# Kernel tuning notes

Hardware: AMD Instinct MI355X
Metric: run time of the kernel (lower is better)

Reference implementation:

```python
import jax, jax.numpy as jnp
import numpy as np

N, NFEAT, NHID, NCLASS = 8192, 128, 128, 40


def _init(key, shape, fan_in):
    return jax.random.normal(key, shape, jnp.float32) / np.sqrt(fan_in).astype(np.float32)


def setup_inputs() -> dict:
    ks = jax.random.split(jax.random.key(0), 8)
    return {
        "x": jax.random.normal(ks[0], (N, NFEAT), jnp.float32),
        # dense normalized adjacency: row-stochastic-ish positive matrix
        "adj": jax.random.uniform(ks[1], (N, N), jnp.float32) * (2.0 / N),
        "W_emb": _init(ks[2], (NFEAT, NHID), NFEAT),
        "b_emb": jnp.zeros((NHID,), jnp.float32),
        "W_gc1": _init(ks[3], (NHID, NHID), NHID),
        "b_gc1": jnp.zeros((NHID,), jnp.float32),
        "W_e": _init(ks[4], (2 * NHID, NHID), 2 * NHID),
        "b_e": jnp.zeros((NHID,), jnp.float32),
        "W_gc2": _init(ks[5], (NHID, NCLASS), NHID),
        "b_gc2": jnp.zeros((NCLASS,), jnp.float32),
        "fully_connected_graph": 1,  # unused by forward (passed but never read)
    }


def reference(x, adj, W_emb, b_emb, W_gc1, b_gc1, W_e, b_e, W_gc2, b_gc2,
              fully_connected_graph):
    nhid = W_emb.shape[1]
    # x = self.emb(x)
    h = x @ W_emb + b_emb  # [N, nhid]

    # Edge branch. Original materializes edge_feat[i*N+j] = concat(h[i], h[j])
    # ([N*N, 2*nhid]) then GraphConvolution_edge: support = edge_feat @ W_e,
    # reshaped [N, N, nhid], aggregated x_e[i] = sum_j adj[i,j] * support[i,j] + b_e.
    # Algebraically identical fused form (same math, no O(N^2*nhid) tensor):
    #   support[i,j] = h[i] @ W_e[:nhid] + h[j] @ W_e[nhid:]
    #   x_e[i] = deg[i] * (h[i] @ W_e_src) + (adj @ (h @ W_e_dst))[i] + b_e
    s_src = h @ W_e[:nhid]   # [N, nhid]
    s_dst = h @ W_e[nhid:]   # [N, nhid]
    deg = adj.sum(axis=1, keepdims=True)  # [N, 1] row sums
    x_e = deg * s_src + adj @ s_dst + b_e  # [N, nhid]

    # Node branch: gc1 -> relu -> dropout(eval: identity) -> gc2 -> log_softmax
    h1 = jax.nn.relu(adj @ (h @ W_gc1) + b_gc1)       # [N, nhid]
    logits = adj @ (h1 @ W_gc2) + b_gc2               # [N, nclass]
    out = jax.nn.log_softmax(logits, axis=1)
    return out, x_e
```

## Files before the change

### kernel.cpp

```cpp
#include <hip/hip_runtime.h>

#define DI __device__ __forceinline__

using f32x4  = __attribute__((ext_vector_type(4))) float;
using bf16x8 = __attribute__((ext_vector_type(8))) __bf16;
using u16x4  = __attribute__((ext_vector_type(4))) unsigned short;
using u32x4  = __attribute__((ext_vector_type(4))) unsigned int;

constexpr int NNODE = 8192;

DI unsigned short f2bf(float f) {
    unsigned int u = __builtin_bit_cast(unsigned int, f);
    u += 0x7fffu + ((u >> 16) & 1u);
    return (unsigned short)(u >> 16);
}
DI float bf2f(unsigned short s) {
    return __builtin_bit_cast(float, (unsigned int)s << 16);
}

DI int swz256(int r, int cb) { return r * 256 + (cb ^ ((r & 15) << 4)); }
DI int swz128(int r, int cb) { return r * 128 + (cb ^ ((r & 7) << 4)); }

__global__ void prep_w(const float* __restrict__ W_emb, const float* __restrict__ W_e,
                       const float* __restrict__ W_gc1, const float* __restrict__ W_gc2,
                       unsigned short* __restrict__ WembT_hi, unsigned short* __restrict__ WembT_lo,
                       unsigned short* __restrict__ WcatT_hi, unsigned short* __restrict__ WcatT_lo,
                       unsigned short* __restrict__ Wg2T_hi, unsigned short* __restrict__ Wg2T_lo)
{
    int gid = blockIdx.x * 256 + threadIdx.x;
    if (gid >= 576 * 128) return;
    int k = gid & 127, n = gid >> 7;
    float v;
    unsigned short *dh, *dl;
    if (n < 128) {
        v = W_emb[k * 128 + n];
        dh = WembT_hi + n * 128 + k; dl = WembT_lo + n * 128 + k;
    } else if (n < 512) {
        int m = n - 128;
        if (m < 128)      v = W_e[k * 128 + m];
        else if (m < 256) v = W_e[(k + 128) * 128 + (m - 128)];
        else              v = W_gc1[k * 128 + (m - 256)];
        dh = WcatT_hi + m * 128 + k; dl = WcatT_lo + m * 128 + k;
    } else {
        int c = n - 512;
        v = (c < 40) ? W_gc2[k * 40 + c] : 0.f;
        dh = Wg2T_hi + c * 128 + k; dl = Wg2T_lo + c * 128 + k;
    }
    unsigned short hi = f2bf(v);
    *dh = hi;
    *dl = f2bf(v - bf2f(hi));
}

__global__ __launch_bounds__(512) void gemm_hs(
    const float* __restrict__ x,
    const unsigned short* __restrict__ WembT_hi, const unsigned short* __restrict__ WembT_lo,
    const unsigned short* __restrict__ WcatT_hi, const unsigned short* __restrict__ WcatT_lo,
    const float* __restrict__ b_emb,
    float* __restrict__ out_s,
    unsigned short* __restrict__ out_t)
{
    __shared__ unsigned short Hh[64 * 128], Hl[64 * 128];
    char* Hhc = (char*)Hh; char* Hlc = (char*)Hl;

    const int tid = threadIdx.x;
    const int r0 = blockIdx.x * 64;
    const int lane = tid & 63, wid = tid >> 6;
    const int lrow = lane & 15, lk8 = (lane >> 4) * 8, lkb = (lane >> 4) * 16;
    const int wrg = wid & 3;
    const int wcg = wid >> 2;

    #pragma unroll
    for (int p = 0; p < 4; ++p) {
        int idx = tid + 512 * p, r = idx >> 5, c4 = idx & 31;
        f32x4 v = *(const f32x4*)(x + (size_t)(r0 + r) * 128 + c4 * 4);
        u16x4 ph, pl;
        #pragma unroll
        for (int j = 0; j < 4; ++j) {
            unsigned short hi = f2bf(v[j]);
            ph[j] = hi; pl[j] = f2bf(v[j] - bf2f(hi));
        }
        *(u16x4*)(Hhc + swz256(r, c4 * 8)) = ph;
        *(u16x4*)(Hlc + swz256(r, c4 * 8)) = pl;
    }
    __syncthreads();

    f32x4 acc[4];
    #pragma unroll
    for (int i = 0; i < 4; ++i) acc[i] = f32x4{0.f, 0.f, 0.f, 0.f};
    const int arow = wrg * 16 + lrow;
    #pragma unroll
    for (int kk = 0; kk < 4; ++kk) {
        bf16x8 ah = *(const bf16x8*)(Hhc + swz256(arow, kk * 64 + lkb));
        bf16x8 al = *(const bf16x8*)(Hlc + swz256(arow, kk * 64 + lkb));
        #pragma unroll
        for (int nf = 0; nf < 4; ++nf) {
            const int n = wcg * 64 + nf * 16 + lrow;
            bf16x8 bh = *(const bf16x8*)(WembT_hi + (size_t)n * 128 + kk * 32 + lk8);
            bf16x8 bl = *(const bf16x8*)(WembT_lo + (size_t)n * 128 + kk * 32 + lk8);
            acc[nf] = __builtin_amdgcn_mfma_f32_16x16x32_bf16(ah, bh, acc[nf], 0, 0, 0);
            acc[nf] = __builtin_amdgcn_mfma_f32_16x16x32_bf16(ah, bl, acc[nf], 0, 0, 0);
            acc[nf] = __builtin_amdgcn_mfma_f32_16x16x32_bf16(al, bh, acc[nf], 0, 0, 0);
        }
    }
    __syncthreads();

    #pragma unroll
    for (int nf = 0; nf < 4; ++nf) {
        const int col = wcg * 64 + nf * 16 + lrow;
        const float bv = b_emb[col];
        #pragma unroll
        for (int j = 0; j < 4; ++j) {
            const int row = wrg * 16 + ((lane >> 4) << 2) + j;
            float v = acc[nf][j] + bv;
            unsigned short hi = f2bf(v);
            *(unsigned short*)(Hhc + swz256(row, col * 2)) = hi;
            *(unsigned short*)(Hlc + swz256(row, col * 2)) = f2bf(v - bf2f(hi));
        }
    }
    __syncthreads();

    f32x4 acc2[12];
    #pragma unroll
    for (int i = 0; i < 12; ++i) acc2[i] = f32x4{0.f, 0.f, 0.f, 0.f};
    #pragma unroll
    for (int kk = 0; kk < 4; ++kk) {
        bf16x8 ah = *(const bf16x8*)(Hhc + swz256(arow, kk * 64 + lkb));
        bf16x8 al = *(const bf16x8*)(Hlc + swz256(arow, kk * 64 + lkb));
        #pragma unroll
        for (int nf = 0; nf < 12; ++nf) {
            const int n = wcg * 192 + nf * 16 + lrow;
            bf16x8 bh = *(const bf16x8*)(WcatT_hi + (size_t)n * 128 + kk * 32 + lk8);
            bf16x8 bl = *(const bf16x8*)(WcatT_lo + (size_t)n * 128 + kk * 32 + lk8);
            acc2[nf] = __builtin_amdgcn_mfma_f32_16x16x32_bf16(ah, bh, acc2[nf], 0, 0, 0);
            acc2[nf] = __builtin_amdgcn_mfma_f32_16x16x32_bf16(ah, bl, acc2[nf], 0, 0, 0);
            acc2[nf] = __builtin_amdgcn_mfma_f32_16x16x32_bf16(al, bh, acc2[nf], 0, 0, 0);
        }
    }
    const int rowb = r0 + wrg * 16 + ((lane >> 4) << 2);
    #pragma unroll
    for (int nf = 0; nf < 12; ++nf) {
        const int col = wcg * 192 + nf * 16 + lrow;
        if (wcg == 0 && nf < 8) {
            #pragma unroll
            for (int j = 0; j < 4; ++j)
                out_s[(size_t)(rowb + j) * 128 + col] = acc2[nf][j];
        } else {
            u16x4 pk = { f2bf(acc2[nf][0]), f2bf(acc2[nf][1]), f2bf(acc2[nf][2]), f2bf(acc2[nf][3]) };
            *(u16x4*)(out_t + (size_t)(col - 128) * NNODE + rowb) = pk;
        }
    }
}

template<int NCOLS, int KSPLIT, bool DEG, bool REV>
__global__ __launch_bounds__(512) void adj_gemm(
    const float* __restrict__ adj,
    const unsigned short* __restrict__ Bt,
    float* __restrict__ Tpart,
    float* __restrict__ degp)
{
    __shared__ unsigned short A_lds[2][64 * 64];
    __shared__ unsigned short B_lds[2][NCOLS * 64];

    const int tid = threadIdx.x;
    const int r0 = blockIdx.x * 64;
    const int ks = blockIdx.y;
    constexpr int KLEN = NNODE / KSPLIT;
    constexpr int NT = KLEN / 64;
    const int kbase = ks * KLEN;

    constexpr int NB = NCOLS / 64;
    f32x4 areg[2];
    u32x4 breg[NB];
    float dsum0 = 0.f, dsum1 = 0.f;
    const int ar0 = tid >> 4, ac4 = tid & 15;

    const int lane = tid & 63, wid = tid >> 6;
    constexpr int FM = (NCOLS == 256) ? 2 : 1;
    constexpr int FN = (NCOLS == 256) ? 4 : 2;
    const int wr = (NCOLS == 256) ? (wid >> 2) : (wid >> 1);
    const int wc = (NCOLS == 256) ? (wid & 3) : (wid & 1);
    const int row_w = wr * FM * 16, col_w = wc * FN * 16;
    const int lrow = lane & 15, lkb = (lane >> 4) * 16;

    f32x4 acc[FM][FN];
    #pragma unroll
    for (int fm = 0; fm < FM; ++fm)
        #pragma unroll
        for (int fn = 0; fn < FN; ++fn) acc[fm][fn] = f32x4{0.f, 0.f, 0.f, 0.f};

    auto order = [&](int tt) { return REV ? (NT - 1 - tt) : tt; };

    auto loadG = [&](int t) {
        const int kt = kbase + t * 64;
        #pragma unroll
        for (int p = 0; p < 2; ++p) {
            areg[p] = *(const f32x4*)(adj + (size_t)(r0 + ar0 + 32 * p) * NNODE + kt + ac4 * 4);
            if (DEG) {
                float s = areg[p][0] + areg[p][1] + areg[p][2] + areg[p][3];
                if (p == 0) dsum0 += s; else dsum1 += s;
            }
        }
        #pragma unroll
        for (int p = 0; p < NB; ++p) {
            const int idx = tid + 512 * p, n = idx >> 3, c = idx & 7;
            breg[p] = *(const u32x4*)(Bt + (size_t)n * NNODE + kt + c * 8);
        }
    };
    auto storeL = [&](int buf) {
        char* Ac = (char*)(A_lds[buf]);
        char* Bc = (char*)(B_lds[buf]);
        #pragma unroll
        for (int p = 0; p < 2; ++p) {
            u16x4 pk = { f2bf(areg[p][0]), f2bf(areg[p][1]), f2bf(areg[p][2]), f2bf(areg[p][3]) };
            *(u16x4*)(Ac + swz128(ar0 + 32 * p, ac4 * 8)) = pk;
        }
        #pragma unroll
        for (int p = 0; p < NB; ++p) {
            const int idx = tid + 512 * p, n = idx >> 3, c = idx & 7;
            *(u32x4*)(Bc + swz128(n, c * 16)) = breg[p];
        }
    };

    loadG(order(0));
    storeL(0);
    for (int tt = 0; tt < NT; ++tt) {
        if (tt + 1 < NT) loadG(order(tt + 1));
        __syncthreads();
        const char* Ac = (const char*)(A_lds[tt & 1]);
        const char* Bc = (const char*)(B_lds[tt & 1]);
        #pragma unroll
        for (int kk = 0; kk < 2; ++kk) {
            bf16x8 a[FM], b[FN];
            #pragma unroll
            for (int fm = 0; fm < FM; ++fm)
                a[fm] = *(const bf16x8*)(Ac + swz128(row_w + fm * 16 + lrow, kk * 64 + lkb));
            #pragma unroll
            for (int fn = 0; fn < FN; ++fn)
                b[fn] = *(const bf16x8*)(Bc + swz128(col_w + fn * 16 + lrow, kk * 64 + lkb));
            #pragma unroll
            for (int fm = 0; fm < FM; ++fm)
                #pragma unroll
                for (int fn = 0; fn < FN; ++fn)
                    acc[fm][fn] = __builtin_amdgcn_mfma_f32_16x16x32_bf16(a[fm], b[fn], acc[fm][fn], 0, 0, 0);
        }
        if (tt + 1 < NT) storeL((tt + 1) & 1);
    }

    float* outp = Tpart + (size_t)ks * NNODE * NCOLS;
    #pragma unroll
    for (int fm = 0; fm < FM; ++fm) {
        const int grow0 = r0 + row_w + fm * 16 + ((lane >> 4) << 2);
        #pragma unroll
        for (int fn = 0; fn < FN; ++fn) {
            const int gcol = col_w + fn * 16 + lrow;
            #pragma unroll
            for (int j = 0; j < 4; ++j)
                outp[(size_t)(grow0 + j) * NCOLS + gcol] = acc[fm][fn][j];
        }
    }

    if (DEG) {
        __syncthreads();
        float* sc = (float*)(&A_lds[0][0]);
        sc[tid] = dsum0;
        sc[512 + tid] = dsum1;
        __syncthreads();
        if (tid < 64) {
            const int base = (tid < 32) ? tid * 16 : (512 + (tid - 32) * 16);
            float s = 0.f;
            #pragma unroll
            for (int i = 0; i < 16; ++i) s += sc[base + i];
            degp[(size_t)ks * NNODE + r0 + tid] = s;
        }
    }
}

template<int KSA>
__global__ __launch_bounds__(256) void post1g2(
    const float* __restrict__ tA,
    const float* __restrict__ s_src,
    const float* __restrict__ degp,
    const float* __restrict__ b_e,
    const float* __restrict__ b_gc1,
    const unsigned short* __restrict__ Wg2T_hi, const unsigned short* __restrict__ Wg2T_lo,
    float* __restrict__ x_e_out,
    unsigned short* __restrict__ out_t)
{
    __shared__ unsigned short Hh[64 * 128], Hl[64 * 128];
    char* Hhc = (char*)Hh; char* Hlc = (char*)Hl;

    const int tid = threadIdx.x;
    const int r0 = blockIdx.x * 64;

    #pragma unroll
    for (int p = 0; p < 8; ++p) {
        int idx = tid + 256 * p, r = idx >> 5, c4 = idx & 31;
        const int gi = r0 + r;
        float dv = 0.f;
        #pragma unroll
        for (int q = 0; q < KSA; ++q) dv += degp[(size_t)q * NNODE + gi];
        f32x4 sdst = f32x4{0.f, 0.f, 0.f, 0.f}, g1 = f32x4{0.f, 0.f, 0.f, 0.f};
        #pragma unroll
        for (int q = 0; q < KSA; ++q) {
            const float* tp = tA + (size_t)q * NNODE * 256 + (size_t)gi * 256;
            f32x4 a = *(const f32x4*)(tp + c4 * 4);
            f32x4 b = *(const f32x4*)(tp + 128 + c4 * 4);
            #pragma unroll
            for (int j = 0; j < 4; ++j) { sdst[j] += a[j]; g1[j] += b[j]; }
        }
        f32x4 ss = *(const f32x4*)(s_src + (size_t)gi * 128 + c4 * 4);
        f32x4 be = *(const f32x4*)(b_e + c4 * 4);
        f32x4 bg = *(const f32x4*)(b_gc1 + c4 * 4);
        f32x4 xe;
        u16x4 ph, pl;
        #pragma unroll
        for (int j = 0; j < 4; ++j) {
            xe[j] = dv * ss[j] + sdst[j] + be[j];
            float h1 = g1[j] + bg[j];
            h1 = h1 > 0.f ? h1 : 0.f;
            unsigned short hi = f2bf(h1);
            ph[j] = hi; pl[j] = f2bf(h1 - bf2f(hi));
        }
        *(f32x4*)(x_e_out + (size_t)gi * 128 + c4 * 4) = xe;
        *(u16x4*)(Hhc + swz256(r, c4 * 8)) = ph;
        *(u16x4*)(Hlc + swz256(r, c4 * 8)) = pl;
    }
    __syncthreads();

    const int lane = tid & 63, wid = tid >> 6;
    const int lrow = lane & 15, lk8 = (lane >> 4) * 8, lkb = (lane >> 4) * 16;
    f32x4 acc[4];
    #pragma unroll
    for (int i = 0; i < 4; ++i) acc[i] = f32x4{0.f, 0.f, 0.f, 0.f};
    const int arow = wid * 16 + lrow;
    #pragma unroll
    for (int kk = 0; kk < 4; ++kk) {
        bf16x8 ah = *(const bf16x8*)(Hhc + swz256(arow, kk * 64 + lkb));
        bf16x8 al = *(const bf16x8*)(Hlc + swz256(arow, kk * 64 + lkb));
        #pragma unroll
        for (int nf = 0; nf < 4; ++nf) {
            const int n = nf * 16 + lrow;
            bf16x8 bh = *(const bf16x8*)(Wg2T_hi + (size_t)n * 128 + kk * 32 + lk8);
            bf16x8 bl = *(const bf16x8*)(Wg2T_lo + (size_t)n * 128 + kk * 32 + lk8);
            acc[nf] = __builtin_amdgcn_mfma_f32_16x16x32_bf16(ah, bh, acc[nf], 0, 0, 0);
            acc[nf] = __builtin_amdgcn_mfma_f32_16x16x32_bf16(ah, bl, acc[nf], 0, 0, 0);
            acc[nf] = __builtin_amdgcn_mfma_f32_16x16x32_bf16(al, bh, acc[nf], 0, 0, 0);
        }
    }
    const int rowb = r0 + wid * 16 + ((lane >> 4) << 2);
    #pragma unroll
    for (int nf = 0; nf < 4; ++nf) {
        const int col = nf * 16 + lrow;
        u16x4 pk = { f2bf(acc[nf][0]), f2bf(acc[nf][1]), f2bf(acc[nf][2]), f2bf(acc[nf][3]) };
        *(u16x4*)(out_t + (size_t)col * NNODE + rowb) = pk;
    }
}

template<int KSPLIT>
__global__ void logsm(const float* __restrict__ tB,
                      const float* __restrict__ b_gc2,
                      float* __restrict__ out)
{
    const int wid = threadIdx.x >> 6, lane = threadIdx.x & 63;
    const int row = blockIdx.x * 4 + wid;
    float v = -1e30f;
    if (lane < 40) {
        float s = b_gc2[lane];
        #pragma unroll
        for (int p = 0; p < KSPLIT; ++p)
            s += tB[(size_t)p * NNODE * 64 + (size_t)row * 64 + lane];
        v = s;
    }
    float m = v;
    #pragma unroll
    for (int off = 32; off; off >>= 1) m = fmaxf(m, __shfl_xor(m, off, 64));
    float e = (lane < 40) ? expf(v - m) : 0.f;
    float s = e;
    #pragma unroll
    for (int off = 32; off; off >>= 1) s += __shfl_xor(s, off, 64);
    if (lane < 40) out[(size_t)row * 40 + lane] = v - m - logf(s);
}

extern "C" void kernel_launch(void* const* d_in, const int* in_sizes, int n_in,
                              void* d_out, int out_size, void* d_ws, size_t ws_size,
                              hipStream_t stream)
{
    const float* x     = (const float*)d_in[0];
    const float* adj   = (const float*)d_in[1];
    const float* W_emb = (const float*)d_in[2];
    const float* b_emb = (const float*)d_in[3];
    const float* W_gc1 = (const float*)d_in[4];
    const float* b_gc1 = (const float*)d_in[5];
    const float* W_e   = (const float*)d_in[6];
    const float* b_e   = (const float*)d_in[7];
    const float* W_gc2 = (const float*)d_in[8];
    const float* b_gc2 = (const float*)d_in[9];

    constexpr int KSA = 2;
    constexpr int KSB = 2;

    char* p = (char*)d_ws;
    auto take = [&](size_t bytes) { char* q = p; p += (bytes + 255) & ~(size_t)255; return q; };

    unsigned short* WembT_hi = (unsigned short*)take(128 * 128 * 2);
    unsigned short* WembT_lo = (unsigned short*)take(128 * 128 * 2);
    unsigned short* WcatT_hi = (unsigned short*)take(384 * 128 * 2);
    unsigned short* WcatT_lo = (unsigned short*)take(384 * 128 * 2);
    unsigned short* Wg2T_hi  = (unsigned short*)take(64 * 128 * 2);
    unsigned short* Wg2T_lo  = (unsigned short*)take(64 * 128 * 2);
    float*          s_src    = (float*)take((size_t)NNODE * 128 * 4);
    unsigned short* B_A      = (unsigned short*)take((size_t)256 * NNODE * 2);
    unsigned short* B_B      = (unsigned short*)take((size_t)64 * NNODE * 2);
    float*          tA       = (float*)take((size_t)KSA * NNODE * 256 * 4);
    float*          tB       = (float*)take((size_t)KSB * NNODE * 64 * 4);
    float*          degp     = (float*)take((size_t)KSA * NNODE * 4);

    float* out_ls = (float*)d_out;
    float* x_e    = (float*)d_out + (size_t)NNODE * 40;

    prep_w<<<288, 256, 0, stream>>>(W_emb, W_e, W_gc1, W_gc2,
                                    WembT_hi, WembT_lo, WcatT_hi, WcatT_lo, Wg2T_hi, Wg2T_lo);
    gemm_hs<<<128, 512, 0, stream>>>(x, WembT_hi, WembT_lo, WcatT_hi, WcatT_lo, b_emb,
                                     s_src, B_A);
    adj_gemm<256, KSA, true, false><<<dim3(128, KSA), 512, 0, stream>>>(adj, B_A, tA, degp);
    post1g2<KSA><<<128, 256, 0, stream>>>(tA, s_src, degp, b_e, b_gc1,
                                          Wg2T_hi, Wg2T_lo, x_e, B_B);
    adj_gemm<64, KSB, false, true><<<dim3(128, KSB), 512, 0, stream>>>(adj, B_B, tB, nullptr);
    logsm<KSB><<<2048, 256, 0, stream>>>(tB, b_gc2, out_ls);
}
```

Baseline: 163.7 us.

## Double register prefetch in adj GEMM with LDS-only barrier

Global loads for the adj GEMM now fill two alternating register sets, so two tiles are in flight instead of one, and the loop is unrolled by two across the LDS double buffer. `__syncthreads` is replaced by a barrier that waits only on LDS counters (`lgkmcnt`), so outstanding global loads are not drained at each barrier. The degree row-sum moves from load time to LDS-store time. This is meant to hide global-memory latency better, at the cost of more vector registers and an assumption that the tile count is even.

New measurement: 174.0 us. 1.06x slower.

```diff
diff --git a/kernel.cpp b/kernel.cpp
--- a/kernel.cpp
+++ b/kernel.cpp
@@ -16,6 +16,12 @@
 }
 DI float bf2f(unsigned short s) {
     return __builtin_bit_cast(float, (unsigned int)s << 16);
+}
+
+DI void lbar() {
+    asm volatile("s_waitcnt lgkmcnt(0)" ::: "memory");
+    __builtin_amdgcn_s_barrier();
+    asm volatile("" ::: "memory");
 }
 
 DI int swz256(int r, int cb) { return r * 256 + (cb ^ ((r & 15) << 4)); }
@@ -169,8 +175,8 @@
     const int kbase = ks * KLEN;
 
     constexpr int NB = NCOLS / 64;
-    f32x4 areg[2];
-    u32x4 breg[NB];
+    struct Regs { f32x4 a[2]; u32x4 b[NB]; };
+    Regs R0, R1;
     float dsum0 = 0.f, dsum1 = 0.f;
     const int ar0 = tid >> 4, ac4 = tid & 15;
 
@@ -190,44 +196,38 @@
 
     auto order = [&](int tt) { return REV ? (NT - 1 - tt) : tt; };
 
-    auto loadG = [&](int t) {
-        const int kt = kbase + t * 64;
+    auto loadG = [&](int t, Regs& R) {
+        const int kt = kbase + order(t) * 64;
+        #pragma unroll
+        for (int p = 0; p < 2; ++p)
+            R.a[p] = *(const f32x4*)(adj + (size_t)(r0 + ar0 + 32 * p) * NNODE + kt + ac4 * 4);
+        #pragma unroll
+        for (int p = 0; p < NB; ++p) {
+            const int idx = tid + 512 * p, n = idx >> 3, c = idx & 7;
+            R.b[p] = *(const u32x4*)(Bt + (size_t)n * NNODE + kt + c * 8);
+        }
+    };
+    auto storeL = [&](int buf, Regs& R) {
+        char* Ac = (char*)(A_lds[buf]);
+        char* Bc = (char*)(B_lds[buf]);
         #pragma unroll
         for (int p = 0; p < 2; ++p) {
-            areg[p] = *(const f32x4*)(adj + (size_t)(r0 + ar0 + 32 * p) * NNODE + kt + ac4 * 4);
             if (DEG) {
-                float s = areg[p][0] + areg[p][1] + areg[p][2] + areg[p][3];
+                float s = R.a[p][0] + R.a[p][1] + R.a[p][2] + R.a[p][3];
                 if (p == 0) dsum0 += s; else dsum1 += s;
             }
+            u16x4 pk = { f2bf(R.a[p][0]), f2bf(R.a[p][1]), f2bf(R.a[p][2]), f2bf(R.a[p][3]) };
+            *(u16x4*)(Ac + swz128(ar0 + 32 * p, ac4 * 8)) = pk;
         }
         #pragma unroll
         for (int p = 0; p < NB; ++p) {
             const int idx = tid + 512 * p, n = idx >> 3, c = idx & 7;
-            breg[p] = *(const u32x4*)(Bt + (size_t)n * NNODE + kt + c * 8);
+            *(u32x4*)(Bc + swz128(n, c * 16)) = R.b[p];
         }
     };
-    auto storeL = [&](int buf) {
-        char* Ac = (char*)(A_lds[buf]);
-        char* Bc = (char*)(B_lds[buf]);
-        #pragma unroll
-        for (int p = 0; p < 2; ++p) {
-            u16x4 pk = { f2bf(areg[p][0]), f2bf(areg[p][1]), f2bf(areg[p][2]), f2bf(areg[p][3]) };
-            *(u16x4*)(Ac + swz128(ar0 + 32 * p, ac4 * 8)) = pk;
-        }
-        #pragma unroll
-        for (int p = 0; p < NB; ++p) {
-            const int idx = tid + 512 * p, n = idx >> 3, c = idx & 7;
-            *(u32x4*)(Bc + swz128(n, c * 16)) = breg[p];
-        }
-    };
-
-    loadG(order(0));
-    storeL(0);
-    for (int tt = 0; tt < NT; ++tt) {
-        if (tt + 1 < NT) loadG(order(tt + 1));
-        __syncthreads();
-        const char* Ac = (const char*)(A_lds[tt & 1]);
-        const char* Bc = (const char*)(B_lds[tt & 1]);
+    auto compute = [&](int buf) {
+        const char* Ac = (const char*)(A_lds[buf]);
+        const char* Bc = (const char*)(B_lds[buf]);
         #pragma unroll
         for (int kk = 0; kk < 2; ++kk) {
             bf16x8 a[FM], b[FN];
@@ -243,7 +243,21 @@
                 for (int fn = 0; fn < FN; ++fn)
                     acc[fm][fn] = __builtin_amdgcn_mfma_f32_16x16x32_bf16(a[fm], b[fn], acc[fm][fn], 0, 0, 0);
         }
-        if (tt + 1 < NT) storeL((tt + 1) & 1);
+    };
+
+    loadG(0, R0);
+    loadG(1, R1);
+    storeL(0, R0);
+    lbar();
+    for (int t = 0; t < NT; t += 2) {
+        if (t + 2 < NT) loadG(t + 2, R0);
+        compute(0);
+        storeL(1, R1);
+        lbar();
+        if (t + 3 < NT) loadG(t + 3, R1);
+        compute(1);
+        if (t + 2 < NT) storeL(0, R0);
+        lbar();
     }
 
     float* outp = Tpart + (size_t)ks * NNODE * NCOLS;
```

## Use direct global-to-LDS async loads with triple buffering in adj GEMM

Applied to the files above, without the earlier changes.

Replaces the register-staged double-buffered load of adj and B tiles with __builtin_amdgcn_global_load_lds DMA into a three-stage LDS ring, issuing loads two tiles ahead and waiting with explicit vmcnt counts. The adj tile now stays in fp32 in LDS and is converted to bf16 at fragment-read time, and the degree row sums are computed from the LDS fragments and reduced with wave shuffles instead of a separate LDS reduction. The aim is to take VGPR staging and conversion off the load path and deepen the prefetch to hide HBM latency. In exchange, LDS use grows (fp32 A, three buffers), which may lower occupancy, and conversion work is repeated per MFMA wave.

After: 222.5 us. 1.36x slower.

```diff
diff --git a/kernel.cpp b/kernel.cpp
--- a/kernel.cpp
+++ b/kernel.cpp
@@ -9,6 +9,9 @@
 
 constexpr int NNODE = 8192;
 
+#define CAST_G(p) (const __attribute__((address_space(1))) unsigned int*)(p)
+#define CAST_S(p) (__attribute__((address_space(3))) unsigned int*)(p)
+
 DI unsigned short f2bf(float f) {
     unsigned int u = __builtin_bit_cast(unsigned int, f);
     u += 0x7fffu + ((u >> 16) & 1u);
@@ -20,6 +23,7 @@
 
 DI int swz256(int r, int cb) { return r * 256 + (cb ^ ((r & 15) << 4)); }
 DI int swz128(int r, int cb) { return r * 128 + (cb ^ ((r & 7) << 4)); }
+DI int swzA(int r, int cb)   { return r * 256 + (cb ^ ((r & 15) << 4)); }
 
 __global__ void prep_w(const float* __restrict__ W_emb, const float* __restrict__ W_e,
                        const float* __restrict__ W_gc1, const float* __restrict__ W_gc2,
@@ -158,98 +162,111 @@
     float* __restrict__ Tpart,
     float* __restrict__ degp)
 {
-    __shared__ unsigned short A_lds[2][64 * 64];
-    __shared__ unsigned short B_lds[2][NCOLS * 64];
+    __shared__ float A_lds[3][64 * 64];
+    __shared__ unsigned short B_lds[3][NCOLS * 64];
 
     const int tid = threadIdx.x;
+    const int lane = tid & 63, wid = tid >> 6;
     const int r0 = blockIdx.x * 64;
     const int ks = blockIdx.y;
     constexpr int KLEN = NNODE / KSPLIT;
     constexpr int NT = KLEN / 64;
     const int kbase = ks * KLEN;
 
-    constexpr int NB = NCOLS / 64;
-    f32x4 areg[2];
-    u32x4 breg[NB];
-    float dsum0 = 0.f, dsum1 = 0.f;
-    const int ar0 = tid >> 4, ac4 = tid & 15;
-
-    const int lane = tid & 63, wid = tid >> 6;
+    constexpr int NBA = 2;
+    constexpr int NBB = NCOLS / 64;
+    constexpr int VM = NBA + NBB;
+
     constexpr int FM = (NCOLS == 256) ? 2 : 1;
     constexpr int FN = (NCOLS == 256) ? 4 : 2;
     const int wr = (NCOLS == 256) ? (wid >> 2) : (wid >> 1);
     const int wc = (NCOLS == 256) ? (wid & 3) : (wid & 1);
     const int row_w = wr * FM * 16, col_w = wc * FN * 16;
-    const int lrow = lane & 15, lkb = (lane >> 4) * 16;
+    const int lrow = lane & 15, g4 = lane >> 4;
 
     f32x4 acc[FM][FN];
     #pragma unroll
     for (int fm = 0; fm < FM; ++fm)
         #pragma unroll
         for (int fn = 0; fn < FN; ++fn) acc[fm][fn] = f32x4{0.f, 0.f, 0.f, 0.f};
-
-    auto order = [&](int tt) { return REV ? (NT - 1 - tt) : tt; };
-
-    auto loadG = [&](int t) {
-        const int kt = kbase + t * 64;
-        #pragma unroll
-        for (int p = 0; p < 2; ++p) {
-            areg[p] = *(const f32x4*)(adj + (size_t)(r0 + ar0 + 32 * p) * NNODE + kt + ac4 * 4);
-            if (DEG) {
-                float s = areg[p][0] + areg[p][1] + areg[p][2] + areg[p][3];
-                if (p == 0) dsum0 += s; else dsum1 += s;
+    float dsum[FM];
+    #pragma unroll
+    for (int fm = 0; fm < FM; ++fm) dsum[fm] = 0.f;
+
+    auto dma = [&](int t, int buf) {
+        const int kt = kbase + (REV ? (NT - 1 - t) : t) * 64;
+        #pragma unroll
+        for (int p = 0; p < NBA; ++p) {
+            const int bidx = wid * 64 + 512 * p;
+            const int idx  = bidx + lane;
+            const int ra   = idx >> 4;
+            const int ce   = ((idx ^ (idx >> 4)) & 15) << 2;
+            __builtin_amdgcn_global_load_lds(
+                CAST_G(adj + (size_t)(r0 + ra) * NNODE + kt + ce),
+                CAST_S(&A_lds[buf][bidx * 4]), 16, 0, 0);
+        }
+        #pragma unroll
+        for (int p = 0; p < NBB; ++p) {
+            const int bidx = wid * 64 + 512 * p;
+            const int idx  = bidx + lane;
+            const int n    = idx >> 3;
+            const int ce   = ((idx ^ (idx >> 3)) & 7) << 3;
+            __builtin_amdgcn_global_load_lds(
+                CAST_G(Bt + (size_t)n * NNODE + kt + ce),
+                CAST_S(&B_lds[buf][bidx * 8]), 16, 0, 0);
+        }
+    };
+
+    auto compute = [&](int buf) {
+        const char* Ac = (const char*)(A_lds[buf]);
+        const char* Bc = (const char*)(B_lds[buf]);
+        #pragma unroll
+        for (int kk = 0; kk < 2; ++kk) {
+            bf16x8 a[FM];
+            #pragma unroll
+            for (int fm = 0; fm < FM; ++fm) {
+                const int r = row_w + fm * 16 + lrow;
+                const int cb0 = kk * 128 + g4 * 32;
+                f32x4 lo = *(const f32x4*)(Ac + swzA(r, cb0));
+                f32x4 hi = *(const f32x4*)(Ac + swzA(r, cb0 + 16));
+                #pragma unroll
+                for (int j = 0; j < 4; ++j) {
+                    a[fm][j]     = __builtin_bit_cast(__bf16, f2bf(lo[j]));
+                    a[fm][4 + j] = __builtin_bit_cast(__bf16, f2bf(hi[j]));
+                }
+                if (DEG && wc == 0)
+                    dsum[fm] += (lo[0] + lo[1] + lo[2] + lo[3]) + (hi[0] + hi[1] + hi[2] + hi[3]);
             }
-        }
-        #pragma unroll
-        for (int p = 0; p < NB; ++p) {
-            const int idx = tid + 512 * p, n = idx >> 3, c = idx & 7;
-            breg[p] = *(const u32x4*)(Bt + (size_t)n * NNODE + kt + c * 8);
-        }
-    };
-    auto storeL = [&](int buf) {
-        char* Ac = (char*)(A_lds[buf]);
-        char* Bc = (char*)(B_lds[buf]);
-        #pragma unroll
-        for (int p = 0; p < 2; ++p) {
-            u16x4 pk = { f2bf(areg[p][0]), f2bf(areg[p][1]), f2bf(areg[p][2]), f2bf(areg[p][3]) };
-            *(u16x4*)(Ac + swz128(ar0 + 32 * p, ac4 * 8)) = pk;
-        }
-        #pragma unroll
-        for (int p = 0; p < NB; ++p) {
-            const int idx = tid + 512 * p, n = idx >> 3, c = idx & 7;
-            *(u32x4*)(Bc + swz128(n, c * 16)) = breg[p];
-        }
-    };
-
-    loadG(order(0));
-    storeL(0);
-    for (int tt = 0; tt < NT; ++tt) {
-        if (tt + 1 < NT) loadG(order(tt + 1));
-        __syncthreads();
-        const char* Ac = (const char*)(A_lds[tt & 1]);
-        const char* Bc = (const char*)(B_lds[tt & 1]);
-        #pragma unroll
-        for (int kk = 0; kk < 2; ++kk) {
-            bf16x8 a[FM], b[FN];
-            #pragma unroll
-            for (int fm = 0; fm < FM; ++fm)
-                a[fm] = *(const bf16x8*)(Ac + swz128(row_w + fm * 16 + lrow, kk * 64 + lkb));
+            bf16x8 b[FN];
             #pragma unroll
             for (int fn = 0; fn < FN; ++fn)
-                b[fn] = *(const bf16x8*)(Bc + swz128(col_w + fn * 16 + lrow, kk * 64 + lkb));
+                b[fn] = *(const bf16x8*)(Bc + swz128(col_w + fn * 16 + lrow, kk * 64 + g4 * 16));
             #pragma unroll
             for (int fm = 0; fm < FM; ++fm)
                 #pragma unroll
                 for (int fn = 0; fn < FN; ++fn)
                     acc[fm][fn] = __builtin_amdgcn_mfma_f32_16x16x32_bf16(a[fm], b[fn], acc[fm][fn], 0, 0, 0);
         }
-        if (tt + 1 < NT) storeL((tt + 1) & 1);
+    };
+
+    dma(0, 0);
+    dma(1, 1);
+    for (int t = 0; t < NT; ++t) {
+        if (t + 1 < NT) {
+            asm volatile("s_waitcnt vmcnt(%0) lgkmcnt(0)" :: "n"(VM) : "memory");
+        } else {
+            asm volatile("s_waitcnt vmcnt(0) lgkmcnt(0)" ::: "memory");
+        }
+        __builtin_amdgcn_s_barrier();
+        asm volatile("" ::: "memory");
+        if (t + 2 < NT) dma(t + 2, (t + 2) % 3);
+        compute(t % 3);
     }
 
     float* outp = Tpart + (size_t)ks * NNODE * NCOLS;
     #pragma unroll
     for (int fm = 0; fm < FM; ++fm) {
-        const int grow0 = r0 + row_w + fm * 16 + ((lane >> 4) << 2);
+        const int grow0 = r0 + row_w + fm * 16 + (g4 << 2);
         #pragma unroll
         for (int fn = 0; fn < FN; ++fn) {
             const int gcol = col_w + fn * 16 + lrow;
@@ -259,18 +276,14 @@
         }
     }
 
-    if (DEG) {
-        __syncthreads();
-        float* sc = (float*)(&A_lds[0][0]);
-        sc[tid] = dsum0;
-        sc[512 + tid] = dsum1;
-        __syncthreads();
-        if (tid < 64) {
-            const int base = (tid < 32) ? tid * 16 : (512 + (tid - 32) * 16);
-            float s = 0.f;
-            #pragma unroll
-            for (int i = 0; i < 16; ++i) s += sc[base + i];
-            degp[(size_t)ks * NNODE + r0 + tid] = s;
+    if (DEG && wc == 0) {
+        #pragma unroll
+        for (int fm = 0; fm < FM; ++fm) {
+            float s = dsum[fm];
+            s += __shfl_xor(s, 16, 64);
+            s += __shfl_xor(s, 32, 64);
+            if (lane < 16)
+                degp[(size_t)ks * NNODE + r0 + row_w + fm * 16 + lane] = s;
         }
     }
 }
```
